# Performance work log

Measured on AMD Instinct MI355X. Metric: run time of the kernel, lower is better.

## Reference

```python
import jax, jax.numpy as jnp
import numpy as np

BN_EPS = 1e-5


def setup_inputs() -> dict:
    key = jax.random.key(0)
    ks = jax.random.split(key, 10)
    B, C, L = 16, 512, 1024
    scale = 1.0 / np.sqrt(C)
    inp = {
        "x": jax.random.normal(ks[0], (B, C, L), dtype=jnp.float32),
        "gamma": jnp.ones((C,), jnp.float32),
        "beta": jnp.zeros((C,), jnp.float32),
        "Wq": jax.random.normal(ks[1], (C, C), jnp.float32) * scale,
        "bq": jnp.zeros((C,), jnp.float32),
        "Wk": jax.random.normal(ks[2], (C, C), jnp.float32) * scale,
        "bk": jnp.zeros((C,), jnp.float32),
        "Wv": jax.random.normal(ks[3], (C, C), jnp.float32) * scale,
        "bv": jnp.zeros((C,), jnp.float32),
        "Wp": jax.random.normal(ks[4], (C, C), jnp.float32) * scale,
        "bp": jnp.zeros((C,), jnp.float32),
    }
    return inp


def _pointwise(W, b, h):
    # Conv1d with kernel_size=1 == per-position linear: [C_out,C_in] x [B,C_in,L]
    return jnp.einsum("oc,bcl->bol", W, h) + b[None, :, None]


def reference(x, gamma, beta, Wq, bq, Wk, bk, Wv, bv, Wp, bp):
    B, C, L = x.shape
    # BatchNorm1d (training-mode batch statistics over batch & length dims)
    mean = jnp.mean(x, axis=(0, 2), keepdims=True)
    var = jnp.var(x, axis=(0, 2), keepdims=True)
    hn = (x - mean) * jax.lax.rsqrt(var + BN_EPS)
    hn = hn * gamma[None, :, None] + beta[None, :, None]

    q = _pointwise(Wq, bq, hn)  # [B,C,L]
    k = _pointwise(Wk, bk, hn)
    v = _pointwise(Wv, bv, hn)

    # attn[b,i,j] = sum_c q[b,c,i] k[b,c,j] / sqrt(C); i=query pos, j=key pos
    attn = jnp.einsum("bci,bcj->bij", q, k) * (C ** -0.5)
    attn = jax.nn.softmax(attn, axis=-1)

    # out[b,c,i] = sum_j attn[b,i,j] v[b,c,j]
    h_ = jnp.einsum("bij,bcj->bci", attn, v)
    h_ = _pointwise(Wp, bp, h_)
    return x + h_
```

## Files before the change

kernel.cpp:

```cpp
#include <hip/hip_runtime.h>
#include <hip/hip_bf16.h>


#define BB 16
#define CC 512
#define LL 1024

typedef __bf16 bf16x8 __attribute__((ext_vector_type(8)));
typedef float  f32x4  __attribute__((ext_vector_type(4)));

__device__ inline unsigned short bf16_bits(float f) {
  __hip_bfloat16 h = __float2bfloat16(f);
  return __builtin_bit_cast(unsigned short, h);
}
__device__ inline float bits_lo(unsigned int u) {
  return __builtin_bit_cast(float, u << 16);
}
__device__ inline float bits_hi(unsigned int u) {
  return __builtin_bit_cast(float, u & 0xffff0000u);
}

__global__ __launch_bounds__(256) void bn_stats(
    const float* __restrict__ x, const float* __restrict__ gamma,
    const float* __restrict__ beta, float* __restrict__ scl,
    float* __restrict__ sft) {
  int c = blockIdx.x;
  int t = threadIdx.x;
  float s = 0.f, s2 = 0.f;
  for (int b = 0; b < BB; ++b) {
    float4 v = ((const float4*)(x + ((size_t)(b * CC + c)) * LL))[t];
    s  += v.x + v.y + v.z + v.w;
    s2 += v.x * v.x + v.y * v.y + v.z * v.z + v.w * v.w;
  }
  for (int m = 32; m; m >>= 1) { s += __shfl_xor(s, m, 64); s2 += __shfl_xor(s2, m, 64); }
  __shared__ float rs[4], rs2[4];
  int wave = t >> 6, lane = t & 63;
  if (lane == 0) { rs[wave] = s; rs2[wave] = s2; }
  __syncthreads();
  if (t == 0) {
    float S  = rs[0] + rs[1] + rs[2] + rs[3];
    float S2 = rs2[0] + rs2[1] + rs2[2] + rs2[3];
    float mean = S * (1.f / 16384.f);
    float var  = S2 * (1.f / 16384.f) - mean * mean;
    float sc = gamma[c] * rsqrtf(var + 1e-5f);
    scl[c] = sc;
    sft[c] = beta[c] - mean * sc;
  }
}

__global__ __launch_bounds__(256) void cast4(
    const float* __restrict__ Wq, const float* __restrict__ Wk,
    const float* __restrict__ Wv, const float* __restrict__ Wp,
    __hip_bfloat16* __restrict__ Wqkv, __hip_bfloat16* __restrict__ Wpb) {
  int m = blockIdx.y;
  const float* src = m == 0 ? Wq : m == 1 ? Wk : m == 2 ? Wv : Wp;
  __hip_bfloat16* dst = m < 3 ? Wqkv + (size_t)m * 262144 : Wpb;
  int i = blockIdx.x * 256 + threadIdx.x;
  float4 v = ((const float4*)src)[i];
  ushort4 o;
  o.x = bf16_bits(v.x); o.y = bf16_bits(v.y);
  o.z = bf16_bits(v.z); o.w = bf16_bits(v.w);
  ((ushort4*)dst)[i] = o;
}

__global__ __launch_bounds__(256) void norm_t(
    const float* __restrict__ x, const float* __restrict__ scl,
    const float* __restrict__ sft, __hip_bfloat16* __restrict__ hnT) {
  __shared__ float tile[32][33];
  int l0 = blockIdx.x * 32, c0 = blockIdx.y * 32, b = blockIdx.z;
  int t = threadIdx.x;
#pragma unroll
  for (int i = 0; i < 4; ++i) {
    int idx = t + i * 256;
    int cc = idx >> 5, ll = idx & 31;
    tile[cc][ll] = x[((size_t)(b * CC + c0 + cc)) * LL + l0 + ll];
  }
  __syncthreads();
#pragma unroll
  for (int i = 0; i < 2; ++i) {
    int idx = t + i * 256;
    int ll = idx >> 4, cc = (idx & 15) * 2;
    float v0 = tile[cc][ll] * scl[c0 + cc] + sft[c0 + cc];
    float v1 = tile[cc + 1][ll] * scl[c0 + cc + 1] + sft[c0 + cc + 1];
    ushort2 o; o.x = bf16_bits(v0); o.y = bf16_bits(v1);
    *(ushort2*)(hnT + ((size_t)(b * LL + l0 + ll)) * CC + c0 + cc) = o;
  }
}

__global__ __launch_bounds__(256) void softmax_bf16(__hip_bfloat16* __restrict__ S) {
  int wave = threadIdx.x >> 6, lane = threadIdx.x & 63;
  size_t row = (size_t)blockIdx.x * 4 + wave;
  uint4* p = (uint4*)(S + row * 1024);
  uint4 r0 = p[lane * 2], r1 = p[lane * 2 + 1];
  float f[16];
  unsigned int w[8] = {r0.x, r0.y, r0.z, r0.w, r1.x, r1.y, r1.z, r1.w};
#pragma unroll
  for (int i = 0; i < 8; ++i) { f[2 * i] = bits_lo(w[i]); f[2 * i + 1] = bits_hi(w[i]); }
  float mx = f[0];
#pragma unroll
  for (int i = 1; i < 16; ++i) mx = fmaxf(mx, f[i]);
  for (int m = 32; m; m >>= 1) mx = fmaxf(mx, __shfl_xor(mx, m, 64));
  float s = 0.f;
#pragma unroll
  for (int i = 0; i < 16; ++i) { f[i] = __expf(f[i] - mx); s += f[i]; }
  for (int m = 32; m; m >>= 1) s += __shfl_xor(s, m, 64);
  float inv = 1.f / s;
  unsigned int ow[8];
#pragma unroll
  for (int i = 0; i < 8; ++i) {
    unsigned int lo = bf16_bits(f[2 * i] * inv);
    unsigned int hi = bf16_bits(f[2 * i + 1] * inv);
    ow[i] = lo | (hi << 16);
  }
  uint4 o0 = {ow[0], ow[1], ow[2], ow[3]}, o1 = {ow[4], ow[5], ow[6], ow[7]};
  p[lane * 2] = o0; p[lane * 2 + 1] = o1;
}

__device__ __forceinline__ void gemm_core(
    const __hip_bfloat16* __restrict__ A, int lda,
    const __hip_bfloat16* __restrict__ B, int ldb, int K,
    __hip_bfloat16* sA, __hip_bfloat16* sB, f32x4 (&acc)[4][4]) {
  const int tid = threadIdx.x;
  const int wave = tid >> 6, lane = tid & 63;
  const int wm = (wave >> 1) * 64, wn = (wave & 1) * 64;
  const int row0 = tid >> 2;
  const int ke0 = (((tid & 3) ^ ((tid >> 3) & 3)) * 8);
  const int fr = lane & 15;
  const int q = lane >> 4;
  const int colA = ((q ^ ((fr >> 1) & 3)) * 8);
  for (int k0 = 0; k0 < K; k0 += 32) {
    __syncthreads();
#pragma unroll
    for (int it = 0; it < 2; ++it) {
      const __hip_bfloat16* ga = A + (size_t)(it * 64 + row0) * lda + (k0 + ke0);
      const __hip_bfloat16* gb = B + (size_t)(it * 64 + row0) * ldb + (k0 + ke0);
      __builtin_amdgcn_global_load_lds(
          (__attribute__((address_space(1))) void*)(void*)ga,
          (__attribute__((address_space(3))) void*)(sA + (it * 256 + wave * 64) * 8),
          16, 0, 0);
      __builtin_amdgcn_global_load_lds(
          (__attribute__((address_space(1))) void*)(void*)gb,
          (__attribute__((address_space(3))) void*)(sB + (it * 256 + wave * 64) * 8),
          16, 0, 0);
    }
    __syncthreads();
    bf16x8 af[4], bfr[4];
#pragma unroll
    for (int i = 0; i < 4; ++i) {
      af[i]  = *(const bf16x8*)(sA + (wm + i * 16 + fr) * 32 + colA);
      bfr[i] = *(const bf16x8*)(sB + (wn + i * 16 + fr) * 32 + colA);
    }
#pragma unroll
    for (int i = 0; i < 4; ++i)
#pragma unroll
      for (int j = 0; j < 4; ++j)
        acc[i][j] = __builtin_amdgcn_mfma_f32_16x16x32_bf16(af[i], bfr[j], acc[i][j], 0, 0, 0);
  }
}

__device__ __forceinline__ void gemm_core256(
    const __hip_bfloat16* __restrict__ A, int lda,
    const __hip_bfloat16* __restrict__ B, int ldb, int K,
    __hip_bfloat16* sA, __hip_bfloat16* sB, f32x4 (&acc)[8][4]) {
  const int tid = threadIdx.x;
  const int wave = tid >> 6, lane = tid & 63;
  const int row0 = tid >> 2;
  const int ke0 = (((tid & 3) ^ ((tid >> 3) & 3)) * 8);
  const int fr = lane & 15;
  const int q = lane >> 4;
  const int colA = ((q ^ ((fr >> 1) & 3)) * 8);
  const int wm = (wave >> 2) * 128, wn = (wave & 3) * 64;
  const int NT = K >> 5;

  const __hip_bfloat16* ga0 = A + (size_t)row0 * lda + ke0;
  const __hip_bfloat16* gb0 = B + (size_t)row0 * ldb + ke0;
  __hip_bfloat16* dA = sA + wave * 512;
  __hip_bfloat16* dB = sB + wave * 512;

#define STAGE256(tt, ss)                                                       \
  {                                                                            \
    const __hip_bfloat16* ga = ga0 + (tt) * 32;                                \
    const __hip_bfloat16* gb = gb0 + (tt) * 32;                                \
    __builtin_amdgcn_global_load_lds(                                          \
        (__attribute__((address_space(1))) void*)(void*)ga,                    \
        (__attribute__((address_space(3))) void*)(dA + (ss) * 8192), 16, 0, 0);\
    __builtin_amdgcn_global_load_lds(                                          \
        (__attribute__((address_space(1))) void*)(void*)(ga + (size_t)128 * lda), \
        (__attribute__((address_space(3))) void*)(dA + (ss) * 8192 + 4096), 16, 0, 0); \
    __builtin_amdgcn_global_load_lds(                                          \
        (__attribute__((address_space(1))) void*)(void*)gb,                    \
        (__attribute__((address_space(3))) void*)(dB + (ss) * 8192), 16, 0, 0);\
    __builtin_amdgcn_global_load_lds(                                          \
        (__attribute__((address_space(1))) void*)(void*)(gb + (size_t)128 * ldb), \
        (__attribute__((address_space(3))) void*)(dB + (ss) * 8192 + 4096), 16, 0, 0); \
  }

  STAGE256(0, 0);
  if (NT > 1) STAGE256(1, 1);
  if (NT > 2) STAGE256(2, 2);

  for (int t = 0; t < NT; ++t) {
    __builtin_amdgcn_sched_barrier(0);
    if (t < NT - 2) {
      asm volatile("s_waitcnt vmcnt(8)" ::: "memory");
    } else if (t == NT - 2) {
      asm volatile("s_waitcnt vmcnt(4)" ::: "memory");
    } else {
      asm volatile("s_waitcnt vmcnt(0)" ::: "memory");
    }
    __builtin_amdgcn_s_barrier();
    __builtin_amdgcn_sched_barrier(0);

    if (t + 3 < NT) STAGE256(t + 3, (t + 3) & 3);

    const __hip_bfloat16* pA = sA + (t & 3) * 8192;
    const __hip_bfloat16* pB = sB + (t & 3) * 8192;
    bf16x8 bfr[4], af0[4], af1[4];
#pragma unroll
    for (int j = 0; j < 4; ++j)
      bfr[j] = *(const bf16x8*)(pB + (wn + j * 16 + fr) * 32 + colA);
#pragma unroll
    for (int i = 0; i < 4; ++i)
      af0[i] = *(const bf16x8*)(pA + (wm + i * 16 + fr) * 32 + colA);
    __builtin_amdgcn_s_setprio(1);
#pragma unroll
    for (int i = 0; i < 4; ++i)
#pragma unroll
      for (int j = 0; j < 4; ++j)
        acc[i][j] = __builtin_amdgcn_mfma_f32_16x16x32_bf16(af0[i], bfr[j], acc[i][j], 0, 0, 0);
    __builtin_amdgcn_s_setprio(0);
#pragma unroll
    for (int i = 0; i < 4; ++i)
      af1[i] = *(const bf16x8*)(pA + (wm + 64 + i * 16 + fr) * 32 + colA);
    __builtin_amdgcn_s_setprio(1);
#pragma unroll
    for (int i = 0; i < 4; ++i)
#pragma unroll
      for (int j = 0; j < 4; ++j)
        acc[4 + i][j] = __builtin_amdgcn_mfma_f32_16x16x32_bf16(af1[i], bfr[j], acc[4 + i][j], 0, 0, 0);
    __builtin_amdgcn_s_setprio(0);
  }
#undef STAGE256
}

__global__ __launch_bounds__(512, 2) void gemm_qkv256(
    const __hip_bfloat16* __restrict__ Wb, const __hip_bfloat16* __restrict__ hnT,
    __hip_bfloat16* __restrict__ qT, __hip_bfloat16* __restrict__ kT,
    __hip_bfloat16* __restrict__ vN,
    const float* __restrict__ bq, const float* __restrict__ bk,
    const float* __restrict__ bv) {
  __shared__ __align__(16) __hip_bfloat16 sA[4 * 8192];
  __shared__ __align__(16) __hip_bfloat16 sB[4 * 8192];
  const int m0 = blockIdx.y * 256, n0 = blockIdx.x * 256;
  f32x4 acc[8][4] = {};
  gemm_core256(Wb + (size_t)m0 * 512, 512, hnT + (size_t)n0 * 512, 512, 512,
               sA, sB, acc);
  const int lane = threadIdx.x & 63, wave = threadIdx.x >> 6;
  const int wm = (wave >> 2) * 128, wn = (wave & 3) * 64;
  const int crow = (lane >> 4) * 4, ccol = lane & 15;
  const int id = m0 >> 9;
  const int mloc0 = (m0 & 511) + wm;
  const float* bias = id == 0 ? bq : id == 1 ? bk : bv;
  if (id < 2) {
    __hip_bfloat16* D = id == 0 ? qT : kT;
#pragma unroll
    for (int i = 0; i < 8; ++i) {
      int mg = mloc0 + i * 16 + crow;
      float bv4[4];
#pragma unroll
      for (int r = 0; r < 4; ++r) bv4[r] = bias[mg + r];
#pragma unroll
      for (int j = 0; j < 4; ++j) {
        size_t ng = (size_t)(n0 + wn + j * 16 + ccol);
        ushort4 o;
        o.x = bf16_bits(acc[i][j][0] + bv4[0]);
        o.y = bf16_bits(acc[i][j][1] + bv4[1]);
        o.z = bf16_bits(acc[i][j][2] + bv4[2]);
        o.w = bf16_bits(acc[i][j][3] + bv4[3]);
        *(ushort4*)(D + ng * 512 + mg) = o;
      }
    }
  } else {
#pragma unroll
    for (int i = 0; i < 8; ++i) {
      int mg = mloc0 + i * 16 + crow;
      float bv4[4];
#pragma unroll
      for (int r = 0; r < 4; ++r) bv4[r] = bias[mg + r];
#pragma unroll
      for (int j = 0; j < 4; ++j) {
        int ngf = n0 + wn + j * 16 + ccol;
        int b = ngf >> 10, l = ngf & 1023;
        __hip_bfloat16* D = vN + ((size_t)b * CC + mg) * LL + l;
#pragma unroll
        for (int r = 0; r < 4; ++r)
          D[(size_t)r * LL] = __float2bfloat16(acc[i][j][r] + bv4[r]);
      }
    }
  }
}

__global__ __launch_bounds__(512, 2) void gemm_s256(
    const __hip_bfloat16* __restrict__ qT, const __hip_bfloat16* __restrict__ kT,
    __hip_bfloat16* __restrict__ Sb) {
  __shared__ __align__(16) __hip_bfloat16 sA[4 * 8192];
  __shared__ __align__(16) __hip_bfloat16 sB[4 * 8192];
  const int bat = blockIdx.z;
  const int m0 = blockIdx.y * 256, n0 = blockIdx.x * 256;
  const size_t sLC = (size_t)LL * CC;
  f32x4 acc[8][4] = {};
  gemm_core256(qT + (size_t)bat * sLC + (size_t)m0 * 512, 512,
               kT + (size_t)bat * sLC + (size_t)n0 * 512, 512, 512,
               sA, sB, acc);
  const int lane = threadIdx.x & 63, wave = threadIdx.x >> 6;
  const int wm = (wave >> 2) * 128, wn = (wave & 3) * 64;
  const int crow = (lane >> 4) * 4, ccol = lane & 15;
  __hip_bfloat16* D = Sb + (size_t)bat * LL * LL;
  const float scale = 0.04419417382415922f;
#pragma unroll
  for (int i = 0; i < 8; ++i) {
    int mg = m0 + wm + i * 16 + crow;
#pragma unroll
    for (int j = 0; j < 4; ++j) {
      int ng = n0 + wn + j * 16 + ccol;
#pragma unroll
      for (int r = 0; r < 4; ++r)
        D[(size_t)(mg + r) * LL + ng] = __float2bfloat16(acc[i][j][r] * scale);
    }
  }
}

template <int MODE, bool BIAS>
__global__ __launch_bounds__(256, 3) void gemm_tn(
    const __hip_bfloat16* __restrict__ A, int lda, size_t strideA,
    const __hip_bfloat16* __restrict__ B, int ldb, size_t strideB,
    void* __restrict__ Dp, int ldd, size_t strideD,
    const float* __restrict__ bias, float scale,
    const float* __restrict__ resid, size_t strideR, int K) {
  __shared__ __align__(16) __hip_bfloat16 sA[128 * 32];
  __shared__ __align__(16) __hip_bfloat16 sB[128 * 32];
  const int bat = blockIdx.z;
  const int m0 = blockIdx.y * 128, n0 = blockIdx.x * 128;
  f32x4 acc[4][4] = {};
  gemm_core(A + (size_t)bat * strideA + (size_t)m0 * lda, lda,
            B + (size_t)bat * strideB + (size_t)n0 * ldb, ldb, K, sA, sB, acc);
  const int lane = threadIdx.x & 63, wave = threadIdx.x >> 6;
  const int wm = (wave >> 1) * 64, wn = (wave & 1) * 64;
  const int crow = (lane >> 4) * 4, ccol = lane & 15;
  if constexpr (MODE == 0) {
    __hip_bfloat16* D = (__hip_bfloat16*)Dp + (size_t)bat * strideD;
#pragma unroll
    for (int i = 0; i < 4; ++i) {
      int mg = m0 + wm + i * 16 + crow;
      float bv4[4];
#pragma unroll
      for (int r = 0; r < 4; ++r) bv4[r] = BIAS ? bias[mg + r] : 0.f;
#pragma unroll
      for (int j = 0; j < 4; ++j) {
        int ng = n0 + wn + j * 16 + ccol;
#pragma unroll
        for (int r = 0; r < 4; ++r)
          D[(size_t)(mg + r) * ldd + ng] =
              __float2bfloat16(acc[i][j][r] * scale + bv4[r]);
      }
    }
  } else {
    float* D = (float*)Dp + (size_t)bat * strideD;
#pragma unroll
    for (int i = 0; i < 4; ++i) {
      int mg = m0 + wm + i * 16 + crow;
      float bv4[4];
#pragma unroll
      for (int r = 0; r < 4; ++r) bv4[r] = BIAS ? bias[mg + r] : 0.f;
#pragma unroll
      for (int j = 0; j < 4; ++j) {
        int ng = n0 + wn + j * 16 + ccol;
        const float* rsrc = resid + (size_t)bat * strideR + (size_t)mg * ldd + ng;
        float* dst = D + (size_t)mg * ldd + ng;
#pragma unroll
        for (int r = 0; r < 4; ++r)
          dst[(size_t)r * ldd] = acc[i][j][r] * scale + bv4[r] + rsrc[(size_t)r * ldd];
      }
    }
  }
}

extern "C" void kernel_launch(void* const* d_in, const int* in_sizes, int n_in,
                              void* d_out, int out_size, void* d_ws, size_t ws_size,
                              hipStream_t stream) {
  const float* x     = (const float*)d_in[0];
  const float* gamma = (const float*)d_in[1];
  const float* beta  = (const float*)d_in[2];
  const float* Wq    = (const float*)d_in[3];
  const float* bq    = (const float*)d_in[4];
  const float* Wk    = (const float*)d_in[5];
  const float* bk    = (const float*)d_in[6];
  const float* Wv    = (const float*)d_in[7];
  const float* bv    = (const float*)d_in[8];
  const float* Wp    = (const float*)d_in[9];
  const float* bp    = (const float*)d_in[10];
  float* out = (float*)d_out;

  char* ws = (char*)d_ws;
  float* scl = (float*)ws;
  float* sft = scl + 512;
  __hip_bfloat16* Wqkvb = (__hip_bfloat16*)(ws + 4096);
  __hip_bfloat16* Wpb = Wqkvb + 786432;
  __hip_bfloat16* hnT = Wpb + 262144;
  __hip_bfloat16* qT  = hnT + 8388608;
  __hip_bfloat16* kT  = qT + 8388608;
  __hip_bfloat16* vN  = kT + 8388608;
  __hip_bfloat16* Sb  = vN + 8388608;
  __hip_bfloat16* HT  = hnT;

  bn_stats<<<512, 256, 0, stream>>>(x, gamma, beta, scl, sft);
  cast4<<<dim3(256, 4), 256, 0, stream>>>(Wq, Wk, Wv, Wp, Wqkvb, Wpb);
  norm_t<<<dim3(32, 16, 16), 256, 0, stream>>>(x, scl, sft, hnT);

  const size_t sLC = (size_t)LL * CC;
  const size_t sCL = (size_t)CC * LL;
  const size_t sLLb = (size_t)LL * LL;

  gemm_qkv256<<<dim3(64, 6), 512, 0, stream>>>(Wqkvb, hnT, qT, kT, vN, bq, bk, bv);
  gemm_s256<<<dim3(4, 4, 16), 512, 0, stream>>>(qT, kT, Sb);
  softmax_bf16<<<4096, 256, 0, stream>>>(Sb);
  gemm_tn<0, false><<<dim3(4, 8, 16), 256, 0, stream>>>(
      Sb, 1024, sLLb, vN, 1024, sCL, HT, 512, sLC, nullptr, 1.f, nullptr, 0, 1024);
  gemm_tn<3, true><<<dim3(8, 4, 16), 256, 0, stream>>>(
      Wpb, 512, 0, HT, 512, sLC, out, 1024, sCL, bp, 1.f, x, sCL, 512);
}
```

Before: 253.6 us.

## Restructure 256x256 GEMM core into 8-phase ping-pong schedule with K=64 tiles

Replaces the 4-stage K=32 global-to-LDS pipeline with a double-buffered K=64 tile loop split into four MFMA phases. Each phase interleaves LDS fragment reads and staged global_load_lds issues, separated by barriers and priority hints. The goal is to overlap memory traffic with matrix-core work and halve loop iterations, in the style of hipBLASLt ping-pong schedules. It adds many extra block barriers per iteration and changes the LDS swizzle to 8-way XOR, which risks synchronization stalls or bank conflicts.

```diff
diff --git a/kernel.cpp b/kernel.cpp
--- a/kernel.cpp
+++ b/kernel.cpp
@@ -158,89 +158,132 @@
   }
 }
 
-__device__ __forceinline__ void gemm_core256(
+__device__ __forceinline__ void gemm_core8p(
     const __hip_bfloat16* __restrict__ A, int lda,
     const __hip_bfloat16* __restrict__ B, int ldb, int K,
     __hip_bfloat16* sA, __hip_bfloat16* sB, f32x4 (&acc)[8][4]) {
   const int tid = threadIdx.x;
   const int wave = tid >> 6, lane = tid & 63;
-  const int row0 = tid >> 2;
-  const int ke0 = (((tid & 3) ^ ((tid >> 3) & 3)) * 8);
-  const int fr = lane & 15;
-  const int q = lane >> 4;
-  const int colA = ((q ^ ((fr >> 1) & 3)) * 8);
+  const int fr = lane & 15, q = lane >> 4;
   const int wm = (wave >> 2) * 128, wn = (wave & 3) * 64;
-  const int NT = K >> 5;
-
-  const __hip_bfloat16* ga0 = A + (size_t)row0 * lda + ke0;
-  const __hip_bfloat16* gb0 = B + (size_t)row0 * ldb + ke0;
-  __hip_bfloat16* dA = sA + wave * 512;
-  __hip_bfloat16* dB = sB + wave * 512;
-
-#define STAGE256(tt, ss)                                                       \
-  {                                                                            \
-    const __hip_bfloat16* ga = ga0 + (tt) * 32;                                \
-    const __hip_bfloat16* gb = gb0 + (tt) * 32;                                \
-    __builtin_amdgcn_global_load_lds(                                          \
-        (__attribute__((address_space(1))) void*)(void*)ga,                    \
-        (__attribute__((address_space(3))) void*)(dA + (ss) * 8192), 16, 0, 0);\
-    __builtin_amdgcn_global_load_lds(                                          \
-        (__attribute__((address_space(1))) void*)(void*)(ga + (size_t)128 * lda), \
-        (__attribute__((address_space(3))) void*)(dA + (ss) * 8192 + 4096), 16, 0, 0); \
-    __builtin_amdgcn_global_load_lds(                                          \
-        (__attribute__((address_space(1))) void*)(void*)gb,                    \
-        (__attribute__((address_space(3))) void*)(dB + (ss) * 8192), 16, 0, 0);\
-    __builtin_amdgcn_global_load_lds(                                          \
-        (__attribute__((address_space(1))) void*)(void*)(gb + (size_t)128 * ldb), \
-        (__attribute__((address_space(3))) void*)(dB + (ss) * 8192 + 4096), 16, 0, 0); \
-  }
-
-  STAGE256(0, 0);
-  if (NT > 1) STAGE256(1, 1);
-  if (NT > 2) STAGE256(2, 2);
+  const int srow = tid >> 3;
+  const int sko = ((tid & 7) ^ (srow & 7)) * 8;
+  const int NT = K >> 6;
+  const int ck0 = (q ^ (fr & 7)) * 8;
+
+#define STG_A(tt, u)                                                           \
+  __builtin_amdgcn_global_load_lds(                                            \
+      (__attribute__((address_space(1))) void*)(void*)(                        \
+          A + (size_t)((u) * 64 + srow) * lda + (tt) * 64 + sko),              \
+      (__attribute__((address_space(3))) void*)(                               \
+          sA + ((tt) & 1) * 16384 + (u) * 4096 + wave * 512), 16, 0, 0)
+#define STG_B(tt, u)                                                           \
+  __builtin_amdgcn_global_load_lds(                                            \
+      (__attribute__((address_space(1))) void*)(void*)(                        \
+          B + (size_t)((u) * 64 + srow) * ldb + (tt) * 64 + sko),              \
+      (__attribute__((address_space(3))) void*)(                               \
+          sB + ((tt) & 1) * 16384 + (u) * 4096 + wave * 512), 16, 0, 0)
+
+  STG_A(0, 0); STG_A(0, 1); STG_A(0, 2); STG_A(0, 3);
+  STG_B(0, 0); STG_B(0, 1); STG_B(0, 2); STG_B(0, 3);
+  STG_A(1, 0); STG_A(1, 1); STG_A(1, 2); STG_A(1, 3);
+  STG_B(1, 0); STG_B(1, 1); STG_B(1, 2); STG_B(1, 3);
 
   for (int t = 0; t < NT; ++t) {
-    __builtin_amdgcn_sched_barrier(0);
-    if (t < NT - 2) {
-      asm volatile("s_waitcnt vmcnt(8)" ::: "memory");
-    } else if (t == NT - 2) {
-      asm volatile("s_waitcnt vmcnt(4)" ::: "memory");
-    } else {
-      asm volatile("s_waitcnt vmcnt(0)" ::: "memory");
-    }
-    __builtin_amdgcn_s_barrier();
-    __builtin_amdgcn_sched_barrier(0);
-
-    if (t + 3 < NT) STAGE256(t + 3, (t + 3) & 3);
-
-    const __hip_bfloat16* pA = sA + (t & 3) * 8192;
-    const __hip_bfloat16* pB = sB + (t & 3) * 8192;
-    bf16x8 bfr[4], af0[4], af1[4];
-#pragma unroll
-    for (int j = 0; j < 4; ++j)
-      bfr[j] = *(const bf16x8*)(pB + (wn + j * 16 + fr) * 32 + colA);
+    const __hip_bfloat16* pA = sA + (t & 1) * 16384;
+    const __hip_bfloat16* pB = sB + (t & 1) * 16384;
+    const int rowA = wm + fr, rowB = wn + fr;
+    const bool st = (t + 2) < NT;
+    bf16x8 a03[4][2], a47[4][2], b01[2][2], b23[2][2];
+
+    __builtin_amdgcn_sched_barrier(0);
+    if (t == NT - 1) { asm volatile("s_waitcnt vmcnt(0)" ::: "memory"); }
+    else             { asm volatile("s_waitcnt vmcnt(8)" ::: "memory"); }
+    __builtin_amdgcn_s_barrier();
+    __builtin_amdgcn_sched_barrier(0);
+
+#pragma unroll
+    for (int i = 0; i < 4; ++i) {
+      a03[i][0] = *(const bf16x8*)(pA + (rowA + i * 16) * 64 + ck0);
+      a03[i][1] = *(const bf16x8*)(pA + (rowA + i * 16) * 64 + (ck0 ^ 32));
+    }
+#pragma unroll
+    for (int j = 0; j < 2; ++j) {
+      b01[j][0] = *(const bf16x8*)(pB + (rowB + j * 16) * 64 + ck0);
+      b01[j][1] = *(const bf16x8*)(pB + (rowB + j * 16) * 64 + (ck0 ^ 32));
+    }
+    __builtin_amdgcn_s_barrier();
+    asm volatile("s_waitcnt lgkmcnt(0)" ::: "memory");
+    __builtin_amdgcn_sched_barrier(0);
+    __builtin_amdgcn_s_setprio(1);
 #pragma unroll
     for (int i = 0; i < 4; ++i)
-      af0[i] = *(const bf16x8*)(pA + (wm + i * 16 + fr) * 32 + colA);
+#pragma unroll
+      for (int j = 0; j < 2; ++j) {
+        acc[i][j] = __builtin_amdgcn_mfma_f32_16x16x32_bf16(a03[i][0], b01[j][0], acc[i][j], 0, 0, 0);
+        acc[i][j] = __builtin_amdgcn_mfma_f32_16x16x32_bf16(a03[i][1], b01[j][1], acc[i][j], 0, 0, 0);
+      }
+    __builtin_amdgcn_s_setprio(0);
+    __builtin_amdgcn_s_barrier();
+    __builtin_amdgcn_sched_barrier(0);
+
+#pragma unroll
+    for (int j = 0; j < 2; ++j) {
+      b23[j][0] = *(const bf16x8*)(pB + (rowB + 32 + j * 16) * 64 + ck0);
+      b23[j][1] = *(const bf16x8*)(pB + (rowB + 32 + j * 16) * 64 + (ck0 ^ 32));
+    }
+    if (st) { STG_A(t + 2, 0); STG_A(t + 2, 2); }
+    __builtin_amdgcn_s_barrier();
+    asm volatile("s_waitcnt lgkmcnt(0)" ::: "memory");
+    __builtin_amdgcn_sched_barrier(0);
     __builtin_amdgcn_s_setprio(1);
 #pragma unroll
     for (int i = 0; i < 4; ++i)
 #pragma unroll
-      for (int j = 0; j < 4; ++j)
-        acc[i][j] = __builtin_amdgcn_mfma_f32_16x16x32_bf16(af0[i], bfr[j], acc[i][j], 0, 0, 0);
+      for (int j = 0; j < 2; ++j) {
+        acc[i][2 + j] = __builtin_amdgcn_mfma_f32_16x16x32_bf16(a03[i][0], b23[j][0], acc[i][2 + j], 0, 0, 0);
+        acc[i][2 + j] = __builtin_amdgcn_mfma_f32_16x16x32_bf16(a03[i][1], b23[j][1], acc[i][2 + j], 0, 0, 0);
+      }
     __builtin_amdgcn_s_setprio(0);
+    __builtin_amdgcn_s_barrier();
+    __builtin_amdgcn_sched_barrier(0);
+
+#pragma unroll
+    for (int i = 0; i < 4; ++i) {
+      a47[i][0] = *(const bf16x8*)(pA + (rowA + 64 + i * 16) * 64 + ck0);
+      a47[i][1] = *(const bf16x8*)(pA + (rowA + 64 + i * 16) * 64 + (ck0 ^ 32));
+    }
+    if (st) { STG_B(t + 2, 0); STG_B(t + 2, 1); STG_B(t + 2, 2); }
+    __builtin_amdgcn_s_barrier();
+    asm volatile("s_waitcnt lgkmcnt(0)" ::: "memory");
+    __builtin_amdgcn_sched_barrier(0);
+    __builtin_amdgcn_s_setprio(1);
 #pragma unroll
     for (int i = 0; i < 4; ++i)
-      af1[i] = *(const bf16x8*)(pA + (wm + 64 + i * 16 + fr) * 32 + colA);
+#pragma unroll
+      for (int j = 0; j < 2; ++j) {
+        acc[4 + i][j] = __builtin_amdgcn_mfma_f32_16x16x32_bf16(a47[i][0], b01[j][0], acc[4 + i][j], 0, 0, 0);
+        acc[4 + i][j] = __builtin_amdgcn_mfma_f32_16x16x32_bf16(a47[i][1], b01[j][1], acc[4 + i][j], 0, 0, 0);
+      }
+    __builtin_amdgcn_s_setprio(0);
+    __builtin_amdgcn_s_barrier();
+    __builtin_amdgcn_sched_barrier(0);
+
+    if (st) { STG_B(t + 2, 3); STG_A(t + 2, 1); STG_A(t + 2, 3); }
+    __builtin_amdgcn_s_barrier();
+    __builtin_amdgcn_sched_barrier(0);
     __builtin_amdgcn_s_setprio(1);
 #pragma unroll
     for (int i = 0; i < 4; ++i)
 #pragma unroll
-      for (int j = 0; j < 4; ++j)
-        acc[4 + i][j] = __builtin_amdgcn_mfma_f32_16x16x32_bf16(af1[i], bfr[j], acc[4 + i][j], 0, 0, 0);
+      for (int j = 0; j < 2; ++j) {
+        acc[4 + i][2 + j] = __builtin_amdgcn_mfma_f32_16x16x32_bf16(a47[i][0], b23[j][0], acc[4 + i][2 + j], 0, 0, 0);
+        acc[4 + i][2 + j] = __builtin_amdgcn_mfma_f32_16x16x32_bf16(a47[i][1], b23[j][1], acc[4 + i][2 + j], 0, 0, 0);
+      }
     __builtin_amdgcn_s_setprio(0);
   }
-#undef STAGE256
+#undef STG_A
+#undef STG_B
 }
 
 __global__ __launch_bounds__(512, 2) void gemm_qkv256(
@@ -249,12 +292,12 @@
     __hip_bfloat16* __restrict__ vN,
     const float* __restrict__ bq, const float* __restrict__ bk,
     const float* __restrict__ bv) {
-  __shared__ __align__(16) __hip_bfloat16 sA[4 * 8192];
-  __shared__ __align__(16) __hip_bfloat16 sB[4 * 8192];
+  __shared__ __align__(16) __hip_bfloat16 sA[2 * 16384];
+  __shared__ __align__(16) __hip_bfloat16 sB[2 * 16384];
   const int m0 = blockIdx.y * 256, n0 = blockIdx.x * 256;
   f32x4 acc[8][4] = {};
-  gemm_core256(Wb + (size_t)m0 * 512, 512, hnT + (size_t)n0 * 512, 512, 512,
-               sA, sB, acc);
+  gemm_core8p(Wb + (size_t)m0 * 512, 512, hnT + (size_t)n0 * 512, 512, 512,
+              sA, sB, acc);
   const int lane = threadIdx.x & 63, wave = threadIdx.x >> 6;
   const int wm = (wave >> 2) * 128, wn = (wave & 3) * 64;
   const int crow = (lane >> 4) * 4, ccol = lane & 15;
@@ -303,15 +346,15 @@
 __global__ __launch_bounds__(512, 2) void gemm_s256(
     const __hip_bfloat16* __restrict__ qT, const __hip_bfloat16* __restrict__ kT,
     __hip_bfloat16* __restrict__ Sb) {
-  __shared__ __align__(16) __hip_bfloat16 sA[4 * 8192];
-  __shared__ __align__(16) __hip_bfloat16 sB[4 * 8192];
+  __shared__ __align__(16) __hip_bfloat16 sA[2 * 16384];
+  __shared__ __align__(16) __hip_bfloat16 sB[2 * 16384];
   const int bat = blockIdx.z;
   const int m0 = blockIdx.y * 256, n0 = blockIdx.x * 256;
   const size_t sLC = (size_t)LL * CC;
   f32x4 acc[8][4] = {};
-  gemm_core256(qT + (size_t)bat * sLC + (size_t)m0 * 512, 512,
-               kT + (size_t)bat * sLC + (size_t)n0 * 512, 512, 512,
-               sA, sB, acc);
+  gemm_core8p(qT + (size_t)bat * sLC + (size_t)m0 * 512, 512,
+              kT + (size_t)bat * sLC + (size_t)n0 * 512, 512, 512,
+              sA, sB, acc);
   const int lane = threadIdx.x & 63, wave = threadIdx.x >> 6;
   const int wm = (wave >> 2) * 128, wn = (wave & 3) * 64;
   const int crow = (lane >> 4) * 4, ccol = lane & 15;
```

After: 242.7 us. 1.05x faster.
